# Performance work log

Hardware: AMD Instinct MI355X
Metric: run time of the kernel (lower is better)

## Reference

```python
import jax, jax.numpy as jnp
import numpy as np


def setup_inputs() -> dict:
    key = jax.random.key(0)
    k_adj, k_ann, k_b = jax.random.split(key, 3)
    B, N, F = 8, 4096, 64
    # Adjacency: sparse-ish nonnegative matrix (TF version stores it as tf.sparse;
    raw = jax.random.uniform(k_adj, (B, N, N), dtype=jnp.float32)
    adjacent = jnp.where(raw > 0.95, raw, 0.0)
    annotations = jax.random.normal(k_ann, (B, N, F), dtype=jnp.float32)
    bias = jax.random.normal(k_b, (1, 1, F), dtype=jnp.float32)
    return {"adjacent": adjacent, "annotations": annotations, "bias": bias}


def reference(adjacent, annotations, bias):
    # Per-batch sparse @ dense matmul in TF == batched matmul here.
    # adjacent: [B,N,N], annotations: [B,N,F] -> [B,N,F]
    out = jnp.einsum('bnm,bmf->bnf', adjacent, annotations)
    return out + bias
```

## Files before the change

kernel.cpp:

```cpp
#include <hip/hip_runtime.h>
#include <stdint.h>

typedef __bf16 bf16x8 __attribute__((ext_vector_type(8)));
typedef float f32x16 __attribute__((ext_vector_type(16)));

#define NN 4096
#define FF 64
#define BM 64
#define BK 64
#define NSTEP (NN / BK)
#define NKB (NN / 16)

__device__ __forceinline__ unsigned short f2bf(float x) {
    unsigned int u = __builtin_bit_cast(unsigned int, x);
    unsigned int r = u + 0x7fffu + ((u >> 16) & 1u);
    return (unsigned short)(r >> 16);
}

__device__ __forceinline__ void gload16(const void* g, void* l) {
    __builtin_amdgcn_global_load_lds((const __attribute__((address_space(1))) void*)g,
                                     (__attribute__((address_space(3))) void*)l, 16, 0, 0);
}

__global__ __launch_bounds__(256) void annP_kernel(const float* __restrict__ ann,
                                                   unsigned short* __restrict__ annP) {
    int blk = blockIdx.x;
    int b = blk >> 6;
    int kb = (blk & 63) * 4 + (threadIdx.x >> 6);
    int f = threadIdx.x & 63;
    const float* src = ann + (size_t)(b * NN + kb * 16) * FF + f;
    unsigned short v[16];
#pragma unroll
    for (int kh = 0; kh < 16; ++kh) v[kh] = f2bf(src[(size_t)kh * FF]);
    unsigned int p[8];
#pragma unroll
    for (int i = 0; i < 8; ++i) p[i] = (unsigned)v[2 * i] | ((unsigned)v[2 * i + 1] << 16);
    uint4* dst = (uint4*)(annP + ((size_t)(b * NKB + kb) * 64 + f) * 16);
    dst[0] = make_uint4(p[0], p[1], p[2], p[3]);
    dst[1] = make_uint4(p[4], p[5], p[6], p[7]);
}

__global__ __launch_bounds__(256, 2) void gconv_kernel(const float* __restrict__ A,
                                                       const unsigned short* __restrict__ annP,
                                                       const float* __restrict__ bias,
                                                       float* __restrict__ out) {
    __shared__ alignas(16) char lds[2][16384];

    int bi = blockIdx.x;
    int b = bi & 7;
    int n0 = (bi >> 3) << 6;
    int t = threadIdx.x, lane = t & 63, wid = t >> 6;
    int wm = wid >> 1, wf = wid & 1;
    int r = lane & 31, h = lane >> 5;

    const float* Ab = A + (size_t)b * NN * NN + (size_t)n0 * NN;

    const float* asrc[4];
#pragma unroll
    for (int j = 0; j < 4; ++j) {
        unsigned s = (unsigned)(wid * 4096 + j * 1024 + lane * 16);
        unsigned row = s >> 8;
        unsigned q = ((s & 255u) ^ ((row & 15u) << 4)) >> 4;
        asrc[j] = Ab + (size_t)row * NN + q * 4;
    }
    auto STAGE = [&](int buf, int k0) {
        char* base = lds[buf];
#pragma unroll
        for (int j = 0; j < 4; ++j) gload16(asrc[j] + k0, base + wid * 4096 + j * 1024);
    };

    const unsigned short* bfp =
        annP + (size_t)b * NKB * 64 * 16 + (size_t)(wf * 32 + r) * 16 + h * 8;

    unsigned abase = (unsigned)((wm * 32 + r) * 256);
    unsigned aswz = (unsigned)(((wm * 32 + r) & 15) << 4);

    f32x16 acc = {};
    uint4 bfrag[4];

    STAGE(0, 0);
#pragma unroll 1
    for (int s = 0; s < NSTEP; ++s) {
        int cur = s & 1;
        int kb0 = s * 4;
#pragma unroll
        for (int kc = 0; kc < 4; ++kc)
            bfrag[kc] = *(const uint4*)(bfp + (size_t)(kb0 + kc) * 1024);
        if (s + 1 < NSTEP) {
            STAGE(cur ^ 1, (s + 1) * BK);
            asm volatile("s_waitcnt vmcnt(8)" ::: "memory");
        } else {
            asm volatile("s_waitcnt vmcnt(4)" ::: "memory");
        }
        __builtin_amdgcn_s_barrier();
        asm volatile("" ::: "memory");

        const char* bufA = lds[cur];
#pragma unroll
        for (int kc = 0; kc < 4; ++kc) {
            unsigned ao = abase + (unsigned)(kc * 64 + h * 32);
            float4 a0 = *(const float4*)(bufA + (ao ^ aswz));
            float4 a1 = *(const float4*)(bufA + ((ao + 16) ^ aswz));
            bf16x8 af = {(__bf16)a0.x, (__bf16)a0.y, (__bf16)a0.z, (__bf16)a0.w,
                         (__bf16)a1.x, (__bf16)a1.y, (__bf16)a1.z, (__bf16)a1.w};
            acc = __builtin_amdgcn_mfma_f32_32x32x16_bf16(
                af, __builtin_bit_cast(bf16x8, bfrag[kc]), acc, 0, 0, 0);
        }
        asm volatile("" ::: "memory");
        __builtin_amdgcn_s_barrier();
        asm volatile("" ::: "memory");
    }

    float bv = bias[wf * 32 + r];
    float* ob = out + ((size_t)(b * NN + n0 + wm * 32)) * FF + wf * 32 + r;
#pragma unroll
    for (int e = 0; e < 16; ++e) {
        int rowl = (e & 3) + 8 * (e >> 2) + h * 4;
        ob[(size_t)rowl * FF] = acc[e] + bv;
    }
}

extern "C" void kernel_launch(void* const* d_in, const int* in_sizes, int n_in,
                              void* d_out, int out_size, void* d_ws, size_t ws_size,
                              hipStream_t stream) {
    const float* adj = (const float*)d_in[0];
    const float* ann = (const float*)d_in[1];
    const float* bias = (const float*)d_in[2];
    float* out = (float*)d_out;
    unsigned short* annP = (unsigned short*)d_ws;

    annP_kernel<<<dim3(8 * 64), dim3(256), 0, stream>>>(ann, annP);
    gconv_kernel<<<dim3(8 * (NN / BM)), dim3(256), 0, stream>>>(adj, annP, bias, out);
}
```

Baseline: 707.7 us.

## Shrink row tile to 32, deepen K tile to 128, use 2-wave blocks with one barrier

Reshapes the GEMM tiling so each block covers 32 output rows with 128-wide K steps, using 128 threads (2 waves) instead of 256, which doubles the grid. The double-buffered pipeline moves to a single barrier per step: wait for all loads, sync, then issue the next stage prefetch after the barrier. The intent is more blocks in flight to saturate HBM bandwidth on the streaming fp32 adjacency read, with fewer barriers per K. In exchange, each annotation fragment is reused across fewer rows, and the full vmcnt(0) wait removes some load/compute overlap.

```diff
diff --git a/kernel.cpp b/kernel.cpp
--- a/kernel.cpp
+++ b/kernel.cpp
@@ -6,8 +6,8 @@
 
 #define NN 4096
 #define FF 64
-#define BM 64
-#define BK 64
+#define BM 32
+#define BK 128
 #define NSTEP (NN / BK)
 #define NKB (NN / 16)
 
@@ -40,79 +40,73 @@
     dst[1] = make_uint4(p[4], p[5], p[6], p[7]);
 }
 
-__global__ __launch_bounds__(256, 2) void gconv_kernel(const float* __restrict__ A,
-                                                       const unsigned short* __restrict__ annP,
-                                                       const float* __restrict__ bias,
-                                                       float* __restrict__ out) {
+__global__ __launch_bounds__(128) void gconv_kernel(const float* __restrict__ A,
+                                                    const unsigned short* __restrict__ annP,
+                                                    const float* __restrict__ bias,
+                                                    float* __restrict__ out) {
     __shared__ alignas(16) char lds[2][16384];
 
     int bi = blockIdx.x;
     int b = bi & 7;
-    int n0 = (bi >> 3) << 6;
-    int t = threadIdx.x, lane = t & 63, wid = t >> 6;
-    int wm = wid >> 1, wf = wid & 1;
+    int n0 = (bi >> 3) << 5;
+    int t = threadIdx.x, lane = t & 63, wf = t >> 6;
     int r = lane & 31, h = lane >> 5;
 
     const float* Ab = A + (size_t)b * NN * NN + (size_t)n0 * NN;
 
-    const float* asrc[4];
+    const float* asrc[8];
 #pragma unroll
-    for (int j = 0; j < 4; ++j) {
-        unsigned s = (unsigned)(wid * 4096 + j * 1024 + lane * 16);
-        unsigned row = s >> 8;
-        unsigned q = ((s & 255u) ^ ((row & 15u) << 4)) >> 4;
+    for (int j = 0; j < 8; ++j) {
+        unsigned s = (unsigned)(j * 2048 + t * 16);
+        unsigned row = s >> 9;
+        unsigned q = ((s & 511u) ^ ((row & 15u) << 4)) >> 4;
         asrc[j] = Ab + (size_t)row * NN + q * 4;
     }
     auto STAGE = [&](int buf, int k0) {
         char* base = lds[buf];
 #pragma unroll
-        for (int j = 0; j < 4; ++j) gload16(asrc[j] + k0, base + wid * 4096 + j * 1024);
+        for (int j = 0; j < 8; ++j) gload16(asrc[j] + k0, base + j * 2048 + wf * 1024);
     };
 
     const unsigned short* bfp =
-        annP + (size_t)b * NKB * 64 * 16 + (size_t)(wf * 32 + r) * 16 + h * 8;
+        annP + (size_t)b * NKB * 1024 + (size_t)(wf * 32 + r) * 16 + h * 8;
 
-    unsigned abase = (unsigned)((wm * 32 + r) * 256);
-    unsigned aswz = (unsigned)(((wm * 32 + r) & 15) << 4);
+    unsigned rbase = (unsigned)(r * 512);
+    unsigned swz = (unsigned)((r & 15) << 4);
 
     f32x16 acc = {};
-    uint4 bfrag[4];
+    uint4 bfrag[8];
 
     STAGE(0, 0);
 #pragma unroll 1
     for (int s = 0; s < NSTEP; ++s) {
         int cur = s & 1;
-        int kb0 = s * 4;
-#pragma unroll
-        for (int kc = 0; kc < 4; ++kc)
-            bfrag[kc] = *(const uint4*)(bfp + (size_t)(kb0 + kc) * 1024);
-        if (s + 1 < NSTEP) {
-            STAGE(cur ^ 1, (s + 1) * BK);
-            asm volatile("s_waitcnt vmcnt(8)" ::: "memory");
-        } else {
-            asm volatile("s_waitcnt vmcnt(4)" ::: "memory");
-        }
+        asm volatile("s_waitcnt vmcnt(0)" ::: "memory");
         __builtin_amdgcn_s_barrier();
         asm volatile("" ::: "memory");
 
+        int kb0 = s * 8;
+#pragma unroll
+        for (int kc = 0; kc < 8; ++kc)
+            bfrag[kc] = *(const uint4*)(bfp + (size_t)(kb0 + kc) * 1024);
+
+        if (s + 1 < NSTEP) STAGE(cur ^ 1, (s + 1) * BK);
+
         const char* bufA = lds[cur];
 #pragma unroll
-        for (int kc = 0; kc < 4; ++kc) {
-            unsigned ao = abase + (unsigned)(kc * 64 + h * 32);
-            float4 a0 = *(const float4*)(bufA + (ao ^ aswz));
-            float4 a1 = *(const float4*)(bufA + ((ao + 16) ^ aswz));
+        for (int kc = 0; kc < 8; ++kc) {
+            unsigned ao = rbase + (unsigned)(kc * 64 + h * 32);
+            float4 a0 = *(const float4*)(bufA + (ao ^ swz));
+            float4 a1 = *(const float4*)(bufA + ((ao + 16) ^ swz));
             bf16x8 af = {(__bf16)a0.x, (__bf16)a0.y, (__bf16)a0.z, (__bf16)a0.w,
                          (__bf16)a1.x, (__bf16)a1.y, (__bf16)a1.z, (__bf16)a1.w};
             acc = __builtin_amdgcn_mfma_f32_32x32x16_bf16(
                 af, __builtin_bit_cast(bf16x8, bfrag[kc]), acc, 0, 0, 0);
         }
-        asm volatile("" ::: "memory");
-        __builtin_amdgcn_s_barrier();
-        asm volatile("" ::: "memory");
     }
 
     float bv = bias[wf * 32 + r];
-    float* ob = out + ((size_t)(b * NN + n0 + wm * 32)) * FF + wf * 32 + r;
+    float* ob = out + ((size_t)(b * NN + n0)) * FF + wf * 32 + r;
 #pragma unroll
     for (int e = 0; e < 16; ++e) {
         int rowl = (e & 3) + 8 * (e >> 2) + h * 4;
@@ -130,5 +124,5 @@
     unsigned short* annP = (unsigned short*)d_ws;
 
     annP_kernel<<<dim3(8 * 64), dim3(256), 0, stream>>>(ann, annP);
-    gconv_kernel<<<dim3(8 * (NN / BM)), dim3(256), 0, stream>>>(adj, annP, bias, out);
+    gconv_kernel<<<dim3(8 * (NN / BM)), dim3(128), 0, stream>>>(adj, annP, bias, out);
 }
```

Measured after the change: 680.4 us (median of 2 runs). -3.9%, faster.
